# Performance work log

Hardware: AMD Instinct MI355X
Metric: run time of the kernel (lower is better)

Reference implementation:

```python
import jax, jax.numpy as jnp
import numpy as np

NHEAD, DK, DV = 8, 32, 32
GRAPH = [[1,2,3,6,7],[1,2,4],[1,3,5],[2,4],[3,5],[1,6,8,12],[1,7,9,13],[6,8,10],[7,9,13],[8,10],[9,11],[9,12,14],[11,13,15],[12,14,16],[13,15,17],[14,16],[15,17]]
_idx = np.zeros((17,5), np.int32); _val = np.zeros((17,5), bool)
for _i, _nb in enumerate(GRAPH):
    for _j, _n in enumerate(_nb):
        _idx[_i,_j] = _n-1; _val[_i,_j] = True
NBR_IDX = jnp.asarray(_idx)            # (17,5) neighbor table (pad idx 0)
NBR_VALID = jnp.asarray(_val)          # (17,5) valid-neighbor mask
ATT_MASK = jnp.asarray(np.concatenate([_val, np.ones((17,2), bool)], 1))  # (17,7): 5 local + 2 global keys
INV_SQRT_DK = float(1.0/np.sqrt(DK))

def _ln_c(x, g, b, eps=1e-6):
    # LayerNorm over channel axis of (B,C,L)
    m = x.mean(1, keepdims=True)
    v = x.var(1, keepdims=True)
    return (x - m) * jax.lax.rsqrt(v + eps) * g[None,:,None] + b[None,:,None]

def _bn3(x, g, b, eps=1e-5):
    # BatchNorm1d (training batch stats) per channel over (B,L); x:(B,C,L)
    m = x.mean((0,2), keepdims=True)
    v = x.var((0,2), keepdims=True)
    return (x - m) * jax.lax.rsqrt(v + eps) * g[None,:,None] + b[None,:,None]

def _pos_ffn(x, w1, b1, w2, b2, g, b):
    # x:(B,C,L); Linear over C, relu, Linear back, residual, BatchNorm1d
    h = jax.nn.relu(jnp.einsum('bcl,hc->bhl', x, w1) + b1[None,:,None])
    y = jnp.einsum('bhl,ch->bcl', h, w2) + b2[None,:,None] + x
    return _bn3(y, g, b)

def _unfold(t):
    # t:(B,C,17) -> (B,C,5,17): per-node 5-wide neighbor window, zero padded
    g = t[:,:,NBR_IDX]                              # (B,C,17,5)
    g = jnp.where(NBR_VALID[None,None], g, 0.0)
    return jnp.transpose(g, (0,1,3,2))

def _sju(xn, ax, wq,bq,wk,bk,wv,bv, bng,bnb, f1w,f1b,f2w,f2b,fg,fb):
    B, C, L = xn.shape
    q = (jnp.einsum('oc,bcl->bol', wq, xn) + bq[None,:,None]).reshape(B,NHEAD,DK,L)
    kx = jnp.einsum('oc,bcl->bol', wk, xn) + bk[None,:,None]
    vx = jnp.einsum('oc,bcl->bol', wv, xn) + bv[None,:,None]
    k = _unfold(kx).reshape(B,NHEAD,DK,5,L)
    v = _unfold(vx).reshape(B,NHEAD,DV,5,L)
    ak = (jnp.einsum('oc,bcal->boal', wk, ax) + bk[None,:,None,None]).reshape(B,NHEAD,DK,2,L)
    av = (jnp.einsum('oc,bcal->boal', wv, ax) + bv[None,:,None,None]).reshape(B,NHEAD,DV,2,L)
    k = jnp.concatenate([k, ak], 3)                 # (B,H,dk,7,L)
    v = jnp.concatenate([v, av], 3)
    pre = jnp.einsum('bhdl,bhdwl->bhwl', q, k) * INV_SQRT_DK
    pre = jnp.where(ATT_MASK.T[None,None], pre, -jnp.inf)
    a = jax.nn.softmax(pre, axis=2)
    att = jnp.einsum('bhwl,bhdwl->bhdl', a, v).reshape(B,C,L)
    ret = _bn3(xn + att, bng, bnb)
    return _pos_ffn(ret, f1w,f1b,f2w,f2b,fg,fb)

def _sru(x, y, wq,bq,wk,bk,wv,bv, bng,bnb, f1w,f1b,f2w,f2b,fg,fb):
    # x:(B,C) relay, y:(B,C,Ly) keys/values
    B, C = x.shape
    q = (x @ wq.T + bq).reshape(B,NHEAD,DK)
    k = (jnp.einsum('oc,bcl->bol', wk, y) + bk[None,:,None]).reshape(B,NHEAD,DK,-1)
    v = (jnp.einsum('oc,bcl->bol', wv, y) + bv[None,:,None]).reshape(B,NHEAD,DV,-1)
    a = jax.nn.softmax(jnp.einsum('bhd,bhdl->bhl', q, k) * INV_SQRT_DK, axis=2)
    att = jnp.einsum('bhl,bhdl->bhd', a, v).reshape(B,C)
    ret = _bn3((x + att)[:,:,None], bng, bnb)
    return _pos_ffn(ret, f1w,f1b,f2w,f2b,fg,fb)[:,:,0]

def _forward(data, ln_g, ln_b, jq_w, jq_b, jk_w, jk_b, jv_w, jv_b, jbn_g, jbn_b, jf1_w, jf1_b, jf2_w, jf2_b, jfbn_g, jfbn_b, rq_w, rq_b, rk_w, rk_b, rv_w, rv_b, rbn_g, rbn_b, rf1_w, rf1_b, rf2_w, rf2_b, rfbn_g, rfbn_b):
    B, C, V, T = data.shape
    embs = jnp.transpose(data, (0,3,1,2)).reshape(B*T, C, V)   # fold time into batch
    nodes = embs
    relay = embs.mean(2)                                       # (BT,C)
    # ax: per node the 2 extra keys = its own original embedding + relay (fixed across layers)
    ax = jnp.stack([embs, jnp.broadcast_to(relay[:,:,None], embs.shape)], axis=2)  # (BT,C,2,V)
    for i in range(ln_g.shape[0]):
        xn = _ln_c(nodes, ln_g[i], ln_b[i])
        nodes = jax.nn.leaky_relu(_sju(xn, ax, jq_w[i],jq_b[i],jk_w[i],jk_b[i],jv_w[i],jv_b[i],jbn_g[i],jbn_b[i],jf1_w[i],jf1_b[i],jf2_w[i],jf2_b[i],jfbn_g[i],jfbn_b[i]), 0.01)
        y = jnp.concatenate([relay[:,:,None], nodes], axis=2)   # (BT,C,18)
        relay = jax.nn.leaky_relu(_sru(relay, y, rq_w[i],rq_b[i],rk_w[i],rk_b[i],rv_w[i],rv_b[i],rbn_g[i],rbn_b[i],rf1_w[i],rf1_b[i],rf2_w[i],rf2_b[i],rfbn_g[i],rfbn_b[i]), 0.01)
    return jnp.transpose(nodes.reshape(B,T,C,V), (0,2,3,1))

def setup_inputs():
    key = jax.random.key(0)
    Lyr, C, DIN, B, T, V = 2, 256, 1024, 4, 256, 17
    ks = jax.random.split(key, 40)
    ctr = [0]
    def nxt():
        k = ks[ctr[0]]; ctr[0] += 1; return k
    def w(shape, s=0.05):
        return jax.random.normal(nxt(), shape, jnp.float32) * s
    ones = lambda: jnp.ones((Lyr, C), jnp.float32)
    zeros = lambda: jnp.zeros((Lyr, C), jnp.float32)
    inp = {'data': jax.random.normal(nxt(), (B,C,V,T), jnp.float32),
           'ln_g': ones(), 'ln_b': zeros()}
    for p in ('j', 'r'):
        inp[p+'q_w'] = w((Lyr,C,C)); inp[p+'q_b'] = w((Lyr,C))
        inp[p+'k_w'] = w((Lyr,C,C)); inp[p+'k_b'] = w((Lyr,C))
        inp[p+'v_w'] = w((Lyr,C,C)); inp[p+'v_b'] = w((Lyr,C))
        inp[p+'bn_g'] = ones(); inp[p+'bn_b'] = zeros()
        inp[p+'f1_w'] = w((Lyr,DIN,C)); inp[p+'f1_b'] = w((Lyr,DIN))
        inp[p+'f2_w'] = w((Lyr,C,DIN)); inp[p+'f2_b'] = w((Lyr,C))
        inp[p+'fbn_g'] = ones(); inp[p+'fbn_b'] = zeros()
    return inp

def reference(data, ln_g, ln_b, jq_w, jq_b, jk_w, jk_b, jv_w, jv_b, jbn_g, jbn_b, jf1_w, jf1_b, jf2_w, jf2_b, jfbn_g, jfbn_b, rq_w, rq_b, rk_w, rk_b, rv_w, rv_b, rbn_g, rbn_b, rf1_w, rf1_b, rf2_w, rf2_b, rfbn_g, rfbn_b):
    return _forward(data, ln_g, ln_b, jq_w, jq_b, jk_w, jk_b, jv_w, jv_b, jbn_g, jbn_b, jf1_w, jf1_b, jf2_w, jf2_b, jfbn_g, jfbn_b, rq_w, rq_b, rk_w, rk_b, rv_w, rv_b, rbn_g, rbn_b, rf1_w, rf1_b, rf2_w, rf2_b, rfbn_g, rfbn_b)
```

## Files before the change

kernel.cpp:

```cpp
#include <hip/hip_runtime.h>
#include <hip/hip_bf16.h>


using bf16 = __hip_bfloat16;
typedef __attribute__((ext_vector_type(8))) short bf16x8v;
typedef __attribute__((ext_vector_type(4))) float f32x4;

namespace {
constexpr int kBT = 1024;
constexpr int kC = 256;
constexpr int kV = 17;
constexpr int kT = 256;
constexpr int kDIN = 1024;
constexpr int kRows = kBT * kV;
constexpr int kRowsE = kRows + kBT;
constexpr float kInvSqrtDk = 0.17677669529663687f;
constexpr size_t SZ_BIG = (size_t)kRows * kC;
}

__constant__ int c_nbi[17][5] = {
    {0, 1, 2, 5, 6},   {0, 1, 3, 0, 0},   {0, 2, 4, 0, 0},  {1, 3, 0, 0, 0},
    {2, 4, 0, 0, 0},   {0, 5, 7, 11, 0},  {0, 6, 8, 12, 0}, {5, 7, 9, 0, 0},
    {6, 8, 12, 0, 0},  {7, 9, 0, 0, 0},   {8, 10, 0, 0, 0}, {8, 11, 13, 0, 0},
    {10, 12, 14, 0, 0},{11, 13, 15, 0, 0},{12, 14, 16, 0, 0},
    {13, 15, 0, 0, 0}, {14, 16, 0, 0, 0}};
__constant__ int c_ncnt[17] = {5, 3, 3, 2, 2, 4, 4, 3, 3, 2, 2, 3, 3, 3, 3, 2, 2};

__device__ inline float bf2f(unsigned short s) {
  unsigned int u = ((unsigned int)s) << 16;
  float f;
  __builtin_memcpy(&f, &u, 4);
  return f;
}
__device__ inline unsigned short f2bf(float f) {
  unsigned int u;
  __builtin_memcpy(&u, &f, 4);
  unsigned int r = (u + 0x7fffu + ((u >> 16) & 1u)) >> 16;
  return (unsigned short)r;
}
__device__ inline float4 ldbf4(const bf16* p) {
  ushort4 u = *(const ushort4*)p;
  return make_float4(bf2f(u.x), bf2f(u.y), bf2f(u.z), bf2f(u.w));
}
__device__ inline void stbf4(bf16* p, float4 v) {
  ushort4 u = make_ushort4(f2bf(v.x), f2bf(v.y), f2bf(v.z), f2bf(v.w));
  *(ushort4*)p = u;
}
__device__ inline float dot4(float4 a, float4 b) {
  return a.x * b.x + a.y * b.y + a.z * b.z + a.w * b.w;
}

__device__ inline void async16(const bf16* g, bf16* l) {
  __builtin_amdgcn_global_load_lds(
      (const __attribute__((address_space(1))) void*)g,
      (__attribute__((address_space(3))) void*)l, 16, 0, 0);
}

template <int KT>
__global__ __launch_bounds__(256, 4) void k_mfma_gemm(
    const bf16* __restrict__ A, const bf16* __restrict__ W,
    const float* __restrict__ bias, const float* __restrict__ res,
    float* __restrict__ outF, bf16* __restrict__ outB,
    const float* __restrict__ bnScI, const float* __restrict__ bnShI,
    float* __restrict__ partOut, int nbPart, int N, int flags) {
  __shared__ __align__(16) char smem_raw[32768];
  bf16* As = (bf16*)smem_raw;
  bf16* Bs = (bf16*)(smem_raw + 16384);
  const int tid = threadIdx.x;
  const int wave = tid >> 6;
  const int lane = tid & 63;
  const int row0 = blockIdx.x * 128;
  const int col0 = blockIdx.y * 128;

  const int sub = lane >> 2;
  const int kq = (lane & 3) * 8;
  const int rg0 = (2 * wave + 0) * 16;
  const int rg1 = (2 * wave + 1) * 16;
  const bf16* ag0 = A + (size_t)(row0 + rg0 + sub) * KT + kq;
  const bf16* ag1 = A + (size_t)(row0 + rg1 + sub) * KT + kq;
  const bf16* bg0 = W + (size_t)(col0 + rg0 + sub) * KT + kq;
  const bf16* bg1 = W + (size_t)(col0 + rg1 + sub) * KT + kq;

  const int wm = wave >> 1, wn = wave & 1;
  const int fr = lane & 15;
  const int fk = (lane >> 4) * 8;

  f32x4 acc[4][4];
#pragma unroll
  for (int i = 0; i < 4; ++i)
#pragma unroll
    for (int j = 0; j < 4; ++j) acc[i][j] = (f32x4){0.f, 0.f, 0.f, 0.f};

#define STAGE32(buf, koff)                              \
  do {                                                  \
    async16(ag0 + (koff), As + (buf) * 4096 + rg0 * 32); \
    async16(ag1 + (koff), As + (buf) * 4096 + rg1 * 32); \
    async16(bg0 + (koff), Bs + (buf) * 4096 + rg0 * 32); \
    async16(bg1 + (koff), Bs + (buf) * 4096 + rg1 * 32); \
  } while (0)

  STAGE32(0, 0);
  __syncthreads();

  for (int k0 = 0; k0 < KT; k0 += 32) {
    const int cur = (k0 >> 5) & 1;
    if (k0 + 32 < KT) STAGE32(cur ^ 1, k0 + 32);
    bf16x8v af[4], bfv[4];
#pragma unroll
    for (int i = 0; i < 4; ++i)
      af[i] = *(const bf16x8v*)&As[cur * 4096 +
                                   (wm * 64 + i * 16 + fr) * 32 + fk];
#pragma unroll
    for (int j = 0; j < 4; ++j)
      bfv[j] = *(const bf16x8v*)&Bs[cur * 4096 +
                                    (wn * 64 + j * 16 + fr) * 32 + fk];
#pragma unroll
    for (int i = 0; i < 4; ++i)
#pragma unroll
      for (int j = 0; j < 4; ++j)
        acc[i][j] = __builtin_amdgcn_mfma_f32_16x16x32_bf16(af[i], bfv[j],
                                                            acc[i][j], 0, 0,
                                                            0);
    __syncthreads();
  }
#undef STAGE32

  if (flags & 4) {
    unsigned short* cs = (unsigned short*)smem_raw;
#pragma unroll
    for (int j = 0; j < 4; ++j) {
      int lc = wn * 64 + j * 16 + fr;
      float bv = bias ? bias[col0 + lc] : 0.f;
#pragma unroll
      for (int i = 0; i < 4; ++i) {
        int lr = wm * 64 + i * 16 + (lane >> 4) * 4;
#pragma unroll
        for (int r = 0; r < 4; ++r) {
          float v = acc[i][j][r] + bv;
          if (flags & 1) v = fmaxf(v, 0.f);
          cs[(lr + r) * 128 + lc] = f2bf(v);
        }
      }
    }
    __syncthreads();
#pragma unroll
    for (int p = 0; p < 8; ++p) {
      int lr = p * 16 + (tid >> 4);
      int lc = (tid & 15) * 8;
      *(bf16x8v*)&outB[(size_t)(row0 + lr) * N + col0 + lc] =
          *(const bf16x8v*)&cs[lr * 128 + lc];
    }
  } else {
    const int crow = row0 + wm * 64;
    const int ccol = col0 + wn * 64;
#pragma unroll
    for (int j = 0; j < 4; ++j) {
      int col = ccol + j * 16 + fr;
      float bv = bias ? bias[col] : 0.f;
      float rsc = 1.f, rsh = 0.f;
      if (flags & 8) { rsc = bnScI[col]; rsh = bnShI[col]; }
#pragma unroll
      for (int i = 0; i < 4; ++i) {
        int rowb = crow + i * 16 + (lane >> 4) * 4;
#pragma unroll
        for (int r = 0; r < 4; ++r) {
          size_t row = (size_t)(rowb + r);
          float v = acc[i][j][r] + bv;
          if (res) v += res[row * N + col] * rsc + rsh;
          if (flags & 1) v = fmaxf(v, 0.f);
          outF[row * N + col] = v;
        }
      }
    }
  }
  (void)partOut; (void)nbPart;
}

__global__ __launch_bounds__(256, 4) void k_mfma_gemm64(
    const bf16* __restrict__ A, const bf16* __restrict__ W,
    const float* __restrict__ bias, const float* __restrict__ res,
    float* __restrict__ outF, const float* __restrict__ bnScI,
    const float* __restrict__ bnShI, float* __restrict__ partOut, int nbPart,
    int N) {
  constexpr int KT = 1024;
  __shared__ __align__(16) bf16 As[2][4096];
  __shared__ __align__(16) bf16 Bs[2][4096];
  __shared__ float sred[4 * 64];
  __shared__ float qred[4 * 64];
  const int tid = threadIdx.x;
  const int wave = tid >> 6;
  const int lane = tid & 63;
  const int row0 = blockIdx.x * 64;
  const int col0 = blockIdx.y * 64;

  const int srow = wave * 16 + (lane >> 2);
  const int skq = (lane & 3) * 8;
  const bf16* ag = A + (size_t)(row0 + srow) * KT + skq;
  const bf16* bg = W + (size_t)(col0 + srow) * KT + skq;

  const int wm = wave >> 1, wn = wave & 1;
  const int fr = lane & 15;
  const int fk = (lane >> 4) * 8;

  f32x4 acc[2][2];
#pragma unroll
  for (int i = 0; i < 2; ++i)
#pragma unroll
    for (int j = 0; j < 2; ++j) acc[i][j] = (f32x4){0.f, 0.f, 0.f, 0.f};

#define STAGE64x64(buf, koff)                                      \
  do {                                                             \
    _Pragma("unroll") for (int kc = 0; kc < 2; ++kc) {             \
      async16(ag + (koff) + kc * 32,                               \
              &As[(buf)][kc * 2048 + wave * 512]);                 \
      async16(bg + (koff) + kc * 32,                               \
              &Bs[(buf)][kc * 2048 + wave * 512]);                 \
    }                                                              \
  } while (0)

  STAGE64x64(0, 0);
  __syncthreads();

  for (int k0 = 0; k0 < KT; k0 += 64) {
    const int cur = (k0 >> 6) & 1;
    if (k0 + 64 < KT) STAGE64x64(cur ^ 1, k0 + 64);
#pragma unroll
    for (int kc = 0; kc < 2; ++kc) {
      bf16x8v af[2], bfv[2];
#pragma unroll
      for (int i = 0; i < 2; ++i)
        af[i] = *(const bf16x8v*)&As[cur][kc * 2048 +
                                          (wm * 32 + i * 16 + fr) * 32 + fk];
#pragma unroll
      for (int j = 0; j < 2; ++j)
        bfv[j] = *(const bf16x8v*)&Bs[cur][kc * 2048 +
                                           (wn * 32 + j * 16 + fr) * 32 + fk];
#pragma unroll
      for (int i = 0; i < 2; ++i)
#pragma unroll
        for (int j = 0; j < 2; ++j)
          acc[i][j] = __builtin_amdgcn_mfma_f32_16x16x32_bf16(af[i], bfv[j],
                                                              acc[i][j], 0, 0,
                                                              0);
    }
    __syncthreads();
  }
#undef STAGE64x64

  const int crow = row0 + wm * 32;
  const int ccol = col0 + wn * 32;
  float colS[2] = {0.f, 0.f};
  float colQ[2] = {0.f, 0.f};
#pragma unroll
  for (int j = 0; j < 2; ++j) {
    int col = ccol + j * 16 + fr;
    float bv = bias[col];
    float rsc = bnScI[col], rsh = bnShI[col];
#pragma unroll
    for (int i = 0; i < 2; ++i) {
      int rowb = crow + i * 16 + (lane >> 4) * 4;
#pragma unroll
      for (int r = 0; r < 4; ++r) {
        size_t row = (size_t)(rowb + r);
        float v = acc[i][j][r] + bv + res[row * N + col] * rsc + rsh;
        outF[row * N + col] = v;
        colS[j] += v;
        colQ[j] += v * v;
      }
    }
  }
#pragma unroll
  for (int j = 0; j < 2; ++j) {
    colS[j] += __shfl_xor(colS[j], 16);
    colS[j] += __shfl_xor(colS[j], 32);
    colQ[j] += __shfl_xor(colQ[j], 16);
    colQ[j] += __shfl_xor(colQ[j], 32);
  }
  if (lane < 16) {
#pragma unroll
    for (int j = 0; j < 2; ++j) {
      sred[wave * 64 + j * 16 + fr] = colS[j];
      qred[wave * 64 + j * 16 + fr] = colQ[j];
    }
  }
  __syncthreads();
  if (tid < 64) {
    int c = tid;
    int wsel = c >> 5, off = c & 31;
    float s = sred[wsel * 64 + off] + sred[(wsel + 2) * 64 + off];
    float q = qred[wsel * 64 + off] + qred[(wsel + 2) * 64 + off];
    int col = col0 + c;
    partOut[(size_t)blockIdx.x * kC + col] = s;
    partOut[(size_t)(nbPart + blockIdx.x) * kC + col] = q;
  }
}

__global__ __launch_bounds__(256) void k_xform_in(const float* __restrict__ data,
                                                  float* __restrict__ nodes,
                                                  bf16* __restrict__ embs_bf) {
  __shared__ float tile[32][33];
  int ct = blockIdx.x * 32, tt = blockIdx.y * 32;
  int bv = blockIdx.z;
  int b = bv / kV, v = bv - b * kV;
  int tx = threadIdx.x & 31, ty = threadIdx.x >> 5;
  for (int i = ty; i < 32; i += 8)
    tile[i][tx] = data[(((size_t)b * kC + ct + i) * kV + v) * kT + tt + tx];
  __syncthreads();
  for (int i = ty; i < 32; i += 8) {
    size_t s = (size_t)b * kT + tt + i;
    size_t idx = (s * kV + v) * kC + ct + tx;
    float val = tile[tx][i];
    nodes[idx] = val;
    embs_bf[idx] = __float2bfloat16(val);
  }
}

__global__ __launch_bounds__(256) void k_xform_out(const float* __restrict__ Z,
                                                   const float* __restrict__ scale,
                                                   const float* __restrict__ shift,
                                                   float* __restrict__ out) {
  __shared__ float tile[32][33];
  int ct = blockIdx.x * 32, tt = blockIdx.y * 32;
  int bv = blockIdx.z;
  int b = bv / kV, v = bv - b * kV;
  int tx = threadIdx.x & 31, ty = threadIdx.x >> 5;
  float sc = scale[ct + tx], sh = shift[ct + tx];
  for (int i = ty; i < 32; i += 8) {
    size_t s = (size_t)b * kT + tt + i;
    float val = Z[(s * kV + v) * kC + ct + tx] * sc + sh;
    val = (val > 0.f) ? val : 0.01f * val;
    tile[i][tx] = val;
  }
  __syncthreads();
  for (int i = ty; i < 32; i += 8)
    out[(((size_t)b * kC + ct + i) * kV + v) * kT + tt + tx] = tile[tx][i];
}

__global__ __launch_bounds__(256) void k_relay_init(const float* __restrict__ nodes,
                                                    bf16* __restrict__ relay0_bf) {
  int t = threadIdx.x;
  int s = blockIdx.x * 4 + (t >> 6);
  int c4 = (t & 63) * 4;
  float4 acc = make_float4(0.f, 0.f, 0.f, 0.f);
#pragma unroll
  for (int v = 0; v < kV; ++v) {
    float4 x = *(const float4*)(nodes + ((size_t)s * kV + v) * kC + c4);
    acc.x += x.x; acc.y += x.y; acc.z += x.z; acc.w += x.w;
  }
  float4 r = make_float4(acc.x / 17.f, acc.y / 17.f, acc.z / 17.f, acc.w / 17.f);
  stbf4(relay0_bf + (size_t)s * kC + c4, r);
}

__global__ __launch_bounds__(256) void k_layernorm(const float* __restrict__ X,
                                                   const float* __restrict__ g,
                                                   const float* __restrict__ b,
                                                   float* __restrict__ O,
                                                   bf16* __restrict__ Ob) {
  int t = threadIdx.x;
  int row = blockIdx.x * 4 + (t >> 6);
  int c4 = (t & 63) * 4;
  size_t i = (size_t)row * kC + c4;
  float4 x = *(const float4*)(X + i);
  float s = x.x + x.y + x.z + x.w;
  float q = dot4(x, x);
#pragma unroll
  for (int o = 32; o >= 1; o >>= 1) {
    s += __shfl_xor(s, o);
    q += __shfl_xor(q, o);
  }
  float m = s * (1.f / 256.f);
  float var = q * (1.f / 256.f) - m * m;
  float rs = rsqrtf(var + 1e-6f);
  float4 g4 = *(const float4*)(g + c4);
  float4 b4 = *(const float4*)(b + c4);
  float4 o4 = make_float4((x.x - m) * rs * g4.x + b4.x,
                          (x.y - m) * rs * g4.y + b4.y,
                          (x.z - m) * rs * g4.z + b4.z,
                          (x.w - m) * rs * g4.w + b4.w);
  *(float4*)(O + i) = o4;
  stbf4(Ob + i, o4);
}

__global__ __launch_bounds__(256) void k_attn_sat(const bf16* __restrict__ qkv,
                                                  const bf16* __restrict__ akav,
                                                  float* __restrict__ z,
                                                  float* __restrict__ part,
                                                  int nb) {
  __shared__ float sS[4][256];
  __shared__ float qS[4][256];
  int t = threadIdx.x;
  int w = t >> 6;
  int rl = blockIdx.x * 4 + w;
  int lane = t & 63;
  int s = rl / kV, l = rl - s * kV;
  int c4 = lane * 4;
  float4 q = ldbf4(qkv + (size_t)rl * 768 + c4);
  int cnt = c_ncnt[l];
  float sc[7];
  int nrow[5];
#pragma unroll
  for (int wd = 0; wd < 5; ++wd) {
    nrow[wd] = s * kV + c_nbi[l][wd];
    float4 k = ldbf4(qkv + (size_t)nrow[wd] * 768 + 256 + c4);
    float p = dot4(q, k);
    p += __shfl_xor(p, 1, 8);
    p += __shfl_xor(p, 2, 8);
    p += __shfl_xor(p, 4, 8);
    sc[wd] = (wd < cnt) ? p * kInvSqrtDk : -1e30f;
  }
  {
    float4 k = ldbf4(akav + (size_t)rl * 1024 + c4);
    float p = dot4(q, k);
    p += __shfl_xor(p, 1, 8);
    p += __shfl_xor(p, 2, 8);
    p += __shfl_xor(p, 4, 8);
    sc[5] = p * kInvSqrtDk;
  }
  {
    float4 k = ldbf4(akav + (size_t)(kRows + s) * 1024 + c4);
    float p = dot4(q, k);
    p += __shfl_xor(p, 1, 8);
    p += __shfl_xor(p, 2, 8);
    p += __shfl_xor(p, 4, 8);
    sc[6] = p * kInvSqrtDk;
  }
  float mx = sc[0];
#pragma unroll
  for (int wd = 1; wd < 7; ++wd) mx = fmaxf(mx, sc[wd]);
  float den = 0.f;
#pragma unroll
  for (int wd = 0; wd < 7; ++wd) {
    sc[wd] = __expf(sc[wd] - mx);
    den += sc[wd];
  }
  float inv = 1.f / den;
  float4 acc = make_float4(0.f, 0.f, 0.f, 0.f);
#pragma unroll
  for (int wd = 0; wd < 5; ++wd) {
    float4 v = ldbf4(qkv + (size_t)nrow[wd] * 768 + 512 + c4);
    acc.x += sc[wd] * v.x; acc.y += sc[wd] * v.y;
    acc.z += sc[wd] * v.z; acc.w += sc[wd] * v.w;
  }
  {
    float4 v = ldbf4(akav + (size_t)rl * 1024 + 256 + c4);
    acc.x += sc[5] * v.x; acc.y += sc[5] * v.y;
    acc.z += sc[5] * v.z; acc.w += sc[5] * v.w;
  }
  {
    float4 v = ldbf4(akav + (size_t)(kRows + s) * 1024 + 256 + c4);
    acc.x += sc[6] * v.x; acc.y += sc[6] * v.y;
    acc.z += sc[6] * v.z; acc.w += sc[6] * v.w;
  }
  size_t zi = (size_t)rl * kC + c4;
  float4 xv = *(const float4*)(z + zi);
  float4 o = make_float4(xv.x + acc.x * inv, xv.y + acc.y * inv,
                         xv.z + acc.z * inv, xv.w + acc.w * inv);
  *(float4*)(z + zi) = o;
  sS[w][c4 + 0] = o.x; sS[w][c4 + 1] = o.y;
  sS[w][c4 + 2] = o.z; sS[w][c4 + 3] = o.w;
  qS[w][c4 + 0] = o.x * o.x; qS[w][c4 + 1] = o.y * o.y;
  qS[w][c4 + 2] = o.z * o.z; qS[w][c4 + 3] = o.w * o.w;
  __syncthreads();
  float ps = sS[0][t] + sS[1][t] + sS[2][t] + sS[3][t];
  float pq = qS[0][t] + qS[1][t] + qS[2][t] + qS[3][t];
  part[(size_t)blockIdx.x * kC + t] = ps;
  part[(size_t)(nb + blockIdx.x) * kC + t] = pq;
}

__global__ __launch_bounds__(256) void k_bn_finalize(const float* __restrict__ part,
                                                     int nb, float inv_n,
                                                     const float* __restrict__ g,
                                                     const float* __restrict__ b,
                                                     float* __restrict__ scale,
                                                     float* __restrict__ shift) {
  int c = blockIdx.x;
  int t = threadIdx.x;
  float s = 0.f, q = 0.f;
  for (int i = t; i < nb; i += 256) {
    s += part[(size_t)i * kC + c];
    q += part[(size_t)(nb + i) * kC + c];
  }
#pragma unroll
  for (int o = 32; o >= 1; o >>= 1) {
    s += __shfl_xor(s, o);
    q += __shfl_xor(q, o);
  }
  __shared__ float ws[4], wq[4];
  int wid = t >> 6;
  if ((t & 63) == 0) { ws[wid] = s; wq[wid] = q; }
  __syncthreads();
  if (t == 0) {
    float S = ws[0] + ws[1] + ws[2] + ws[3];
    float Q = wq[0] + wq[1] + wq[2] + wq[3];
    float m = S * inv_n;
    float var = Q * inv_n - m * m;
    float sc = g[c] * rsqrtf(var + 1e-5f);
    scale[c] = sc;
    shift[c] = b[c] - m * sc;
  }
}

__global__ __launch_bounds__(256) void k_bn_apply(const float* __restrict__ Z,
                                                  const float* __restrict__ scale,
                                                  const float* __restrict__ shift,
                                                  float* __restrict__ outF,
                                                  bf16* __restrict__ outB,
                                                  int leaky) {
  int t = threadIdx.x;
  int row = blockIdx.x * 4 + (t >> 6);
  int c4 = (t & 63) * 4;
  size_t i = (size_t)row * kC + c4;
  float4 z = *(const float4*)(Z + i);
  float4 sc = *(const float4*)(scale + c4);
  float4 sh = *(const float4*)(shift + c4);
  float4 v = make_float4(z.x * sc.x + sh.x, z.y * sc.y + sh.y,
                         z.z * sc.z + sh.z, z.w * sc.w + sh.w);
  if (leaky) {
    v.x = (v.x > 0.f) ? v.x : 0.01f * v.x;
    v.y = (v.y > 0.f) ? v.y : 0.01f * v.y;
    v.z = (v.z > 0.f) ? v.z : 0.01f * v.z;
    v.w = (v.w > 0.f) ? v.w : 0.01f * v.w;
  }
  if (outF) *(float4*)(outF + i) = v;
  if (outB) stbf4(outB + i, v);
}

__global__ __launch_bounds__(256) void k_bn_ln(
    const float* __restrict__ Z, const float* __restrict__ scale,
    const float* __restrict__ shift, const float* __restrict__ g,
    const float* __restrict__ b, float* __restrict__ xnOut,
    bf16* __restrict__ actOut) {
  int t = threadIdx.x;
  int row = blockIdx.x * 4 + (t >> 6);
  int c4 = (t & 63) * 4;
  size_t i = (size_t)row * kC + c4;
  float4 z = *(const float4*)(Z + i);
  float4 sc = *(const float4*)(scale + c4);
  float4 sh = *(const float4*)(shift + c4);
  float4 v = make_float4(z.x * sc.x + sh.x, z.y * sc.y + sh.y,
                         z.z * sc.z + sh.z, z.w * sc.w + sh.w);
  v.x = (v.x > 0.f) ? v.x : 0.01f * v.x;
  v.y = (v.y > 0.f) ? v.y : 0.01f * v.y;
  v.z = (v.z > 0.f) ? v.z : 0.01f * v.z;
  v.w = (v.w > 0.f) ? v.w : 0.01f * v.w;
  float s = v.x + v.y + v.z + v.w;
  float q = dot4(v, v);
#pragma unroll
  for (int o = 32; o >= 1; o >>= 1) {
    s += __shfl_xor(s, o);
    q += __shfl_xor(q, o);
  }
  float m = s * (1.f / 256.f);
  float var = q * (1.f / 256.f) - m * m;
  float rs = rsqrtf(var + 1e-6f);
  float4 g4 = *(const float4*)(g + c4);
  float4 b4 = *(const float4*)(b + c4);
  float4 o4 = make_float4((v.x - m) * rs * g4.x + b4.x,
                          (v.y - m) * rs * g4.y + b4.y,
                          (v.z - m) * rs * g4.z + b4.z,
                          (v.w - m) * rs * g4.w + b4.w);
  *(float4*)(xnOut + i) = o4;
  stbf4(actOut + i, o4);
}

struct CvtTab {
  const float* src[12];
  bf16* dst[12];
  int n[12];
  const float* bsrc[10];
  float* bdst[10];
};
__global__ __launch_bounds__(256) void k_cvt_multi(CvtTab t) {
  int c = blockIdx.y;
  if (c == 12) {
    if (blockIdx.x < 10) t.bdst[blockIdx.x][threadIdx.x] = t.bsrc[blockIdx.x][threadIdx.x];
    return;
  }
  int i = (blockIdx.x * 256 + threadIdx.x) * 4;
  if (i >= t.n[c]) return;
  float4 v = *(const float4*)(t.src[c] + i);
  stbf4(t.dst[c] + i, v);
}

extern "C" void kernel_launch(void* const* d_in, const int* in_sizes, int n_in,
                              void* d_out, int out_size, void* d_ws, size_t ws_size,
                              hipStream_t stream) {
  const float* data = (const float*)d_in[0];
  const float* ln_g = (const float*)d_in[1];
  const float* ln_b = (const float*)d_in[2];
  const float* jq_w = (const float*)d_in[3];
  const float* jq_b = (const float*)d_in[4];
  const float* jk_w = (const float*)d_in[5];
  const float* jk_b = (const float*)d_in[6];
  const float* jv_w = (const float*)d_in[7];
  const float* jv_b = (const float*)d_in[8];
  const float* jbn_g = (const float*)d_in[9];
  const float* jbn_b = (const float*)d_in[10];
  const float* jf1_w = (const float*)d_in[11];
  const float* jf1_b = (const float*)d_in[12];
  const float* jf2_w = (const float*)d_in[13];
  const float* jf2_b = (const float*)d_in[14];
  const float* jfbn_g = (const float*)d_in[15];
  const float* jfbn_b = (const float*)d_in[16];
  float* out = (float*)d_out;

  float* f = (float*)d_ws;
  float* nodes = f;    f += SZ_BIG;
  float* xn = f;       f += SZ_BIG;
  float* part = f;     f += 2 * (kRows / 4) * kC;
  float* scale = f;    f += kC;
  float* shift = f;    f += kC;
  float* cb_jqkv = f;  f += 2 * 768;
  float* cb_kv4 = f;   f += 1024;

  bf16* bfa = (bf16*)f;
  bf16* act_bf = bfa;   bfa += SZ_BIG;
  bf16* embsX_bf = bfa; bfa += (size_t)kRowsE * kC;
  bf16* P = bfa;        bfa += (size_t)kRows * kDIN;
  bf16* akavBuf = bfa;  bfa += (size_t)kRowsE * 1024;
  bf16* Wjqkv = bfa;    bfa += 2 * 768 * 256;
  bf16* Wkv4 = bfa;     bfa += 1024 * 256;
  bf16* Wjf1 = bfa;     bfa += 2 * 1024 * 256;
  bf16* Wjf2 = bfa;     bfa += 2 * 256 * 1024;

  bf16* relay0_bf = embsX_bf + SZ_BIG;
  bf16* qkv_bf = P;
  bf16* h_bf = P;
  float* y2 = xn;

  auto gemm = [&](const bf16* A, const bf16* W, const float* bias,
                  bf16* oB, int M, int N, int K, int flags) {
    dim3 g(M / 128, N / 128);
    if (K == 256)
      k_mfma_gemm<256><<<g, 256, 0, stream>>>(A, W, bias, nullptr, nullptr,
                                              oB, nullptr, nullptr, nullptr, 0,
                                              N, flags);
    else
      k_mfma_gemm<1024><<<g, 256, 0, stream>>>(A, W, bias, nullptr, nullptr,
                                               oB, nullptr, nullptr, nullptr,
                                               0, N, flags);
  };

  {
    CvtTab t;
    for (int i = 0; i < 2; ++i) {
      const size_t om = (size_t)i * kC * kC;
      const float* s3[3] = {jq_w + om, jk_w + om, jv_w + om};
      bf16* d3[3] = {Wjqkv + (size_t)i * 768 * 256,
                     Wjqkv + (size_t)i * 768 * 256 + 65536,
                     Wjqkv + (size_t)i * 768 * 256 + 131072};
      for (int j = 0; j < 3; ++j) {
        t.src[i * 3 + j] = s3[j];
        t.dst[i * 3 + j] = d3[j];
        t.n[i * 3 + j] = 65536;
      }
    }
    t.src[6] = jk_w;                 t.dst[6] = Wkv4;               t.n[6] = 65536;
    t.src[7] = jv_w;                 t.dst[7] = Wkv4 + 65536;       t.n[7] = 65536;
    t.src[8] = jk_w + (size_t)65536; t.dst[8] = Wkv4 + 131072;      t.n[8] = 65536;
    t.src[9] = jv_w + (size_t)65536; t.dst[9] = Wkv4 + 196608;      t.n[9] = 65536;
    t.src[10] = jf1_w; t.dst[10] = Wjf1; t.n[10] = 2 * 1024 * 256;
    t.src[11] = jf2_w; t.dst[11] = Wjf2; t.n[11] = 2 * 256 * 1024;
    for (int i = 0; i < 2; ++i) {
      t.bsrc[i * 3 + 0] = jq_b + (size_t)i * kC;
      t.bsrc[i * 3 + 1] = jk_b + (size_t)i * kC;
      t.bsrc[i * 3 + 2] = jv_b + (size_t)i * kC;
      t.bdst[i * 3 + 0] = cb_jqkv + i * 768;
      t.bdst[i * 3 + 1] = cb_jqkv + i * 768 + 256;
      t.bdst[i * 3 + 2] = cb_jqkv + i * 768 + 512;
    }
    t.bsrc[6] = jk_b;       t.bdst[6] = cb_kv4;
    t.bsrc[7] = jv_b;       t.bdst[7] = cb_kv4 + 256;
    t.bsrc[8] = jk_b + kC;  t.bdst[8] = cb_kv4 + 512;
    t.bsrc[9] = jv_b + kC;  t.bdst[9] = cb_kv4 + 768;
    k_cvt_multi<<<dim3(512, 13), 256, 0, stream>>>(t);
  }

  k_xform_in<<<dim3(8, 8, 4 * kV), 256, 0, stream>>>(data, nodes, embsX_bf);
  k_relay_init<<<kBT / 4, 256, 0, stream>>>(nodes, relay0_bf);

  gemm(embsX_bf, Wkv4, cb_kv4, akavBuf, kRowsE, 1024, 256, 4);

  k_layernorm<<<kRows / 4, 256, 0, stream>>>(nodes, ln_g, ln_b, xn, act_bf);

  for (int i = 0; i < 2; ++i) {
    const size_t ob = (size_t)i * kC, ofb1 = (size_t)i * kDIN;
    const bf16* Wj = Wjqkv + (size_t)i * 768 * 256;
    const bf16* Wf1 = Wjf1 + (size_t)i * 1024 * 256;
    const bf16* Wf2 = Wjf2 + (size_t)i * 256 * 1024;
    const float* cbj = cb_jqkv + i * 768;
    const int nbA = kRows / 4;
    const int nbG = kRows / 64;

    gemm(act_bf, Wj, cbj, qkv_bf, kRows, 768, 256, 4);
    k_attn_sat<<<kRows / 4, 256, 0, stream>>>(qkv_bf, akavBuf + (size_t)i * 512,
                                              xn, part, nbA);
    k_bn_finalize<<<kC, 256, 0, stream>>>(part, nbA, 1.f / kRows, jbn_g + ob,
                                          jbn_b + ob, scale, shift);
    k_bn_apply<<<kRows / 4, 256, 0, stream>>>(xn, scale, shift, nullptr,
                                              act_bf, 0);
    gemm(act_bf, Wf1, jf1_b + ofb1, h_bf, kRows, 1024, 256, 4 | 1);
    k_mfma_gemm64<<<dim3(kRows / 64, kC / 64), 256, 0, stream>>>(
        h_bf, Wf2, jf2_b + ob, xn, y2, scale, shift, part, nbG, kC);
    k_bn_finalize<<<kC, 256, 0, stream>>>(part, nbG, 1.f / kRows, jfbn_g + ob,
                                          jfbn_b + ob, scale, shift);
    if (i == 0) {
      k_bn_ln<<<kRows / 4, 256, 0, stream>>>(y2, scale, shift, ln_g + kC,
                                             ln_b + kC, xn, act_bf);
    }
  }

  k_xform_out<<<dim3(8, 8, 4 * kV), 256, 0, stream>>>(y2, scale, shift, out);
  (void)in_sizes; (void)n_in; (void)out_size; (void)ws_size;
}
```

Before: 407.3 us.

## Load GEMM operands directly from global into registers, dropping LDS staging

The K=256 MFMA GEMM no longer stages A and W tiles through LDS with async global-to-LDS loads and per-step barriers. Each wave now loads its MFMA fragments straight from global memory into registers, double-buffered in two register sets with sched_barriers so the next chunk's loads are in flight while the current chunk's MFMAs run. The aim is to remove LDS traffic and __syncthreads overhead. The cost is that fragments shared between waves are fetched from global/L2 twice instead of once, and register pressure rises, so launch bounds drop from 4 to 3 blocks; unused template and epilogue paths are also removed.

After: 503.1 us. 23.5% more time.

```diff
diff --git a/kernel.cpp b/kernel.cpp
--- a/kernel.cpp
+++ b/kernel.cpp
@@ -56,74 +56,61 @@
       (__attribute__((address_space(3))) void*)l, 16, 0, 0);
 }
 
-template <int KT>
-__global__ __launch_bounds__(256, 4) void k_mfma_gemm(
+__global__ __launch_bounds__(256, 3) void k_mfma_gemm(
     const bf16* __restrict__ A, const bf16* __restrict__ W,
-    const float* __restrict__ bias, const float* __restrict__ res,
-    float* __restrict__ outF, bf16* __restrict__ outB,
-    const float* __restrict__ bnScI, const float* __restrict__ bnShI,
-    float* __restrict__ partOut, int nbPart, int N, int flags) {
+    const float* __restrict__ bias, bf16* __restrict__ outB, int N,
+    int flags) {
+  constexpr int KT = 256;
   __shared__ __align__(16) char smem_raw[32768];
-  bf16* As = (bf16*)smem_raw;
-  bf16* Bs = (bf16*)(smem_raw + 16384);
   const int tid = threadIdx.x;
   const int wave = tid >> 6;
   const int lane = tid & 63;
   const int row0 = blockIdx.x * 128;
   const int col0 = blockIdx.y * 128;
 
-  const int sub = lane >> 2;
-  const int kq = (lane & 3) * 8;
-  const int rg0 = (2 * wave + 0) * 16;
-  const int rg1 = (2 * wave + 1) * 16;
-  const bf16* ag0 = A + (size_t)(row0 + rg0 + sub) * KT + kq;
-  const bf16* ag1 = A + (size_t)(row0 + rg1 + sub) * KT + kq;
-  const bf16* bg0 = W + (size_t)(col0 + rg0 + sub) * KT + kq;
-  const bf16* bg1 = W + (size_t)(col0 + rg1 + sub) * KT + kq;
-
   const int wm = wave >> 1, wn = wave & 1;
   const int fr = lane & 15;
   const int fk = (lane >> 4) * 8;
 
+  const bf16* Abase = A + (size_t)(row0 + wm * 64 + fr) * KT + fk;
+  const bf16* Bbase = W + (size_t)(col0 + wn * 64 + fr) * KT + fk;
+
   f32x4 acc[4][4];
 #pragma unroll
   for (int i = 0; i < 4; ++i)
 #pragma unroll
     for (int j = 0; j < 4; ++j) acc[i][j] = (f32x4){0.f, 0.f, 0.f, 0.f};
 
-#define STAGE32(buf, koff)                              \
-  do {                                                  \
-    async16(ag0 + (koff), As + (buf) * 4096 + rg0 * 32); \
-    async16(ag1 + (koff), As + (buf) * 4096 + rg1 * 32); \
-    async16(bg0 + (koff), Bs + (buf) * 4096 + rg0 * 32); \
-    async16(bg1 + (koff), Bs + (buf) * 4096 + rg1 * 32); \
+  bf16x8v a0[4], b0[4], a1[4], b1[4];
+
+#define LOADSTAGE(ar, br, kcc)                                            \
+  do {                                                                    \
+    _Pragma("unroll") for (int i = 0; i < 4; ++i) {                       \
+      ar[i] = *(const bf16x8v*)(Abase + (size_t)(i * 16) * KT + (kcc) * 32); \
+      br[i] = *(const bf16x8v*)(Bbase + (size_t)(i * 16) * KT + (kcc) * 32); \
+    }                                                                     \
   } while (0)
 
-  STAGE32(0, 0);
-  __syncthreads();
-
-  for (int k0 = 0; k0 < KT; k0 += 32) {
-    const int cur = (k0 >> 5) & 1;
-    if (k0 + 32 < KT) STAGE32(cur ^ 1, k0 + 32);
-    bf16x8v af[4], bfv[4];
-#pragma unroll
-    for (int i = 0; i < 4; ++i)
-      af[i] = *(const bf16x8v*)&As[cur * 4096 +
-                                   (wm * 64 + i * 16 + fr) * 32 + fk];
-#pragma unroll
-    for (int j = 0; j < 4; ++j)
-      bfv[j] = *(const bf16x8v*)&Bs[cur * 4096 +
-                                    (wn * 64 + j * 16 + fr) * 32 + fk];
-#pragma unroll
-    for (int i = 0; i < 4; ++i)
-#pragma unroll
-      for (int j = 0; j < 4; ++j)
-        acc[i][j] = __builtin_amdgcn_mfma_f32_16x16x32_bf16(af[i], bfv[j],
-                                                            acc[i][j], 0, 0,
-                                                            0);
-    __syncthreads();
-  }
-#undef STAGE32
+#define MFMAG(ar, br)                                                     \
+  do {                                                                    \
+    _Pragma("unroll") for (int i = 0; i < 4; ++i)                         \
+        _Pragma("unroll") for (int j = 0; j < 4; ++j) acc[i][j] =         \
+            __builtin_amdgcn_mfma_f32_16x16x32_bf16(ar[i], br[j],         \
+                                                    acc[i][j], 0, 0, 0);  \
+  } while (0)
+
+  LOADSTAGE(a0, b0, 0);
+#pragma unroll
+  for (int kc = 0; kc < 8; kc += 2) {
+    LOADSTAGE(a1, b1, kc + 1);
+    __builtin_amdgcn_sched_barrier(0);
+    MFMAG(a0, b0);
+    if (kc + 2 < 8) LOADSTAGE(a0, b0, kc + 2);
+    __builtin_amdgcn_sched_barrier(0);
+    MFMAG(a1, b1);
+  }
+#undef LOADSTAGE
+#undef MFMAG
 
   if (flags & 4) {
     unsigned short* cs = (unsigned short*)smem_raw;
@@ -150,30 +137,7 @@
       *(bf16x8v*)&outB[(size_t)(row0 + lr) * N + col0 + lc] =
           *(const bf16x8v*)&cs[lr * 128 + lc];
     }
-  } else {
-    const int crow = row0 + wm * 64;
-    const int ccol = col0 + wn * 64;
-#pragma unroll
-    for (int j = 0; j < 4; ++j) {
-      int col = ccol + j * 16 + fr;
-      float bv = bias ? bias[col] : 0.f;
-      float rsc = 1.f, rsh = 0.f;
-      if (flags & 8) { rsc = bnScI[col]; rsh = bnShI[col]; }
-#pragma unroll
-      for (int i = 0; i < 4; ++i) {
-        int rowb = crow + i * 16 + (lane >> 4) * 4;
-#pragma unroll
-        for (int r = 0; r < 4; ++r) {
-          size_t row = (size_t)(rowb + r);
-          float v = acc[i][j][r] + bv;
-          if (res) v += res[row * N + col] * rsc + rsh;
-          if (flags & 1) v = fmaxf(v, 0.f);
-          outF[row * N + col] = v;
-        }
-      }
-    }
-  }
-  (void)partOut; (void)nbPart;
+  }
 }
 
 __global__ __launch_bounds__(256, 4) void k_mfma_gemm64(
@@ -629,16 +593,9 @@
   float* y2 = xn;
 
   auto gemm = [&](const bf16* A, const bf16* W, const float* bias,
-                  bf16* oB, int M, int N, int K, int flags) {
+                  bf16* oB, int M, int N, int flags) {
     dim3 g(M / 128, N / 128);
-    if (K == 256)
-      k_mfma_gemm<256><<<g, 256, 0, stream>>>(A, W, bias, nullptr, nullptr,
-                                              oB, nullptr, nullptr, nullptr, 0,
-                                              N, flags);
-    else
-      k_mfma_gemm<1024><<<g, 256, 0, stream>>>(A, W, bias, nullptr, nullptr,
-                                               oB, nullptr, nullptr, nullptr,
-                                               0, N, flags);
+    k_mfma_gemm<<<g, 256, 0, stream>>>(A, W, bias, oB, N, flags);
   };
 
   {
@@ -679,7 +636,7 @@
   k_xform_in<<<dim3(8, 8, 4 * kV), 256, 0, stream>>>(data, nodes, embsX_bf);
   k_relay_init<<<kBT / 4, 256, 0, stream>>>(nodes, relay0_bf);
 
-  gemm(embsX_bf, Wkv4, cb_kv4, akavBuf, kRowsE, 1024, 256, 4);
+  gemm(embsX_bf, Wkv4, cb_kv4, akavBuf, kRowsE, 1024, 4);
 
   k_layernorm<<<kRows / 4, 256, 0, stream>>>(nodes, ln_g, ln_b, xn, act_bf);
 
@@ -692,14 +649,14 @@
     const int nbA = kRows / 4;
     const int nbG = kRows / 64;
 
-    gemm(act_bf, Wj, cbj, qkv_bf, kRows, 768, 256, 4);
+    gemm(act_bf, Wj, cbj, qkv_bf, kRows, 768, 4);
     k_attn_sat<<<kRows / 4, 256, 0, stream>>>(qkv_bf, akavBuf + (size_t)i * 512,
                                               xn, part, nbA);
     k_bn_finalize<<<kC, 256, 0, stream>>>(part, nbA, 1.f / kRows, jbn_g + ob,
                                           jbn_b + ob, scale, shift);
     k_bn_apply<<<kRows / 4, 256, 0, stream>>>(xn, scale, shift, nullptr,
                                               act_bf, 0);
-    gemm(act_bf, Wf1, jf1_b + ofb1, h_bf, kRows, 1024, 256, 4 | 1);
+    gemm(act_bf, Wf1, jf1_b + ofb1, h_bf, kRows, 1024, 4 | 1);
     k_mfma_gemm64<<<dim3(kRows / 64, kC / 64), 256, 0, stream>>>(
         h_bf, Wf2, jf2_b + ob, xn, y2, scale, shift, part, nbG, kC);
     k_bn_finalize<<<kC, 256, 0, stream>>>(part, nbG, 1.f / kRows, jfbn_g + ob,
```
